# Optimization experiments

Hardware: AMD Instinct MI355X
Metric: run time of the kernel (lower is better)

## Reference

```python
import jax, jax.numpy as jnp
import numpy as np

B, D_W, D_C, D_P = 4096, 2048, 1024, 2048
RANK = D_W // 4  # 512, per A_U/A_V shapes (d_w, d_w//4)


def setup_inputs() -> dict:
    key = jax.random.key(0)
    ks = jax.random.split(key, 10)
    return {
        "w_prev": jax.random.normal(ks[0], (B, D_W), jnp.float32),
        "z_t": jax.random.normal(ks[1], (B, D_P), jnp.float32),
        "c_t": jax.random.normal(ks[2], (B, D_C), jnp.float32),
        # params (mirroring flax init: A_diag zeros, A_U/A_V normal(0.01),
        # Dense kernels lecun_normal-ish scale, zero biases)
        "A_diag": jnp.zeros((D_W,), jnp.float32),
        "A_U": 0.01 * jax.random.normal(ks[3], (D_W, RANK), jnp.float32),
        "A_V": 0.01 * jax.random.normal(ks[4], (D_W, RANK), jnp.float32),
        "W_mod": jax.random.normal(ks[5], (D_C, D_W), jnp.float32) / np.sqrt(D_C),
        "b_mod": jnp.zeros((D_W,), jnp.float32),
        "W_B": jax.random.normal(ks[6], (D_C + D_P, D_W), jnp.float32) / np.sqrt(D_C + D_P),
        "b_B": jnp.zeros((D_W,), jnp.float32),
    }


def reference(w_prev, z_t, c_t, A_diag, A_U, A_V, W_mod, b_mod, W_B, b_B):
    # A = diag(tanh(A_diag)*0.9) + A_U @ A_V^T, row-scaled by modulation.
    # Equivalent (same math) without materializing [B, d_w, d_w]:
    #   (A * m[:, :, None]) @ w = m * (a_diag * w + A_U @ (A_V^T @ w))
    a_diag = jnp.tanh(A_diag) * 0.9                              # [d_w]
    modulation = jnp.tanh(c_t @ W_mod + b_mod)                   # [B, d_w]
    Aw = a_diag * w_prev + (w_prev @ A_V) @ A_U.T                # [B, d_w]
    Bt = jnp.concatenate([c_t, z_t], axis=-1) @ W_B + b_B        # [B, d_w]
    return modulation * Aw + Bt
```

## Files before the change

### kernel.cpp

```cpp
#include <hip/hip_runtime.h>


#define DEV __device__ __forceinline__

typedef __bf16 v8bf __attribute__((ext_vector_type(8)));
typedef __bf16 v4bf __attribute__((ext_vector_type(4)));
typedef float  v4f  __attribute__((ext_vector_type(4)));

typedef __attribute__((address_space(1))) const unsigned int* as1_cuint_ptr;
typedef __attribute__((address_space(3))) unsigned int*       as3_uint_ptr;

DEV void async16(const void* g, void* l) {
  __builtin_amdgcn_global_load_lds(
      (as1_cuint_ptr)(unsigned long long)g,
      (as3_uint_ptr)(unsigned long long)l,
      16, 0, 0);
}

DEV float tanh_fast(float x) {
  x = fminf(15.f, fmaxf(-15.f, x));
  float e = __expf(2.f * x);
  return (e - 1.f) / (e + 1.f);
}

__global__ __launch_bounds__(256, 2) void prep_gemm(
    const float* __restrict__ w, const float* __restrict__ z,
    const float* __restrict__ c, const float* __restrict__ au,
    const float* __restrict__ av, const float* __restrict__ Wmod,
    const float* __restrict__ WB, const float* __restrict__ A_diag,
    __bf16* __restrict__ wb, __bf16* __restrict__ zb, __bf16* __restrict__ cb,
    __bf16* __restrict__ Wmodt, __bf16* __restrict__ WBt,
    __bf16* __restrict__ Mt) {
  __shared__ __align__(16) char smem[16384];
  int b = blockIdx.x;

  if (b < 256) {
    __bf16* As = (__bf16*)smem;
    __bf16* Bs = (__bf16*)(smem + 8192);
    const int tid = threadIdx.x, lane = tid & 63, wid = tid >> 6;
    const int wm = wid >> 1, wn = wid & 1, l16 = lane & 15, quad = lane >> 4;
    const int m0 = (b >> 4) * 128, n0 = (b & 15) * 128;
    const int qs = quad ^ ((l16 >> 1) & 3);
    const int row = tid >> 1, sp = (tid & 1) * 2;

    v4f acc[4][4];
#pragma unroll
    for (int i = 0; i < 4; ++i)
#pragma unroll
      for (int j = 0; j < 4; ++j) { v4f zz = {0, 0, 0, 0}; acc[i][j] = zz; }

    for (int k0 = 0; k0 < 512; k0 += 32) {
      __syncthreads();
#pragma unroll
      for (int ss = 0; ss < 2; ++ss) {
        const int s = sp + ss;
        const int gk = (s ^ ((row >> 1) & 3)) * 8;
        const float* pa = au + (size_t)(m0 + row) * 512 + k0 + gk;
        const float* pb = av + (size_t)(n0 + row) * 512 + k0 + gk;
        float4 a0 = *reinterpret_cast<const float4*>(pa);
        float4 a1 = *reinterpret_cast<const float4*>(pa + 4);
        float4 b0 = *reinterpret_cast<const float4*>(pb);
        float4 b1 = *reinterpret_cast<const float4*>(pb + 4);
        v8bf va, vb;
        va[0] = (__bf16)a0.x; va[1] = (__bf16)a0.y;
        va[2] = (__bf16)a0.z; va[3] = (__bf16)a0.w;
        va[4] = (__bf16)a1.x; va[5] = (__bf16)a1.y;
        va[6] = (__bf16)a1.z; va[7] = (__bf16)a1.w;
        vb[0] = (__bf16)b0.x; vb[1] = (__bf16)b0.y;
        vb[2] = (__bf16)b0.z; vb[3] = (__bf16)b0.w;
        vb[4] = (__bf16)b1.x; vb[5] = (__bf16)b1.y;
        vb[6] = (__bf16)b1.z; vb[7] = (__bf16)b1.w;
        *reinterpret_cast<v8bf*>(&As[row * 32 + s * 8]) = va;
        *reinterpret_cast<v8bf*>(&Bs[row * 32 + s * 8]) = vb;
      }
      __syncthreads();
      const v8bf* Ap = reinterpret_cast<const v8bf*>(As);
      const v8bf* Bp = reinterpret_cast<const v8bf*>(Bs);
      v8bf a[4], bb[4];
#pragma unroll
      for (int i = 0; i < 4; ++i) a[i] = Ap[(wm * 64 + i * 16 + l16) * 4 + qs];
#pragma unroll
      for (int j = 0; j < 4; ++j) bb[j] = Bp[(wn * 64 + j * 16 + l16) * 4 + qs];
#pragma unroll
      for (int i = 0; i < 4; ++i)
#pragma unroll
        for (int j = 0; j < 4; ++j)
          acc[i][j] = __builtin_amdgcn_mfma_f32_16x16x32_bf16(a[i], bb[j],
                                                              acc[i][j], 0, 0, 0);
    }

    const int mBase = m0 + wm * 64 + quad * 4;
    const int nBase = n0 + wn * 64 + l16;
#pragma unroll
    for (int j = 0; j < 4; ++j) {
      const int n = nBase + j * 16;
#pragma unroll
      for (int i = 0; i < 4; ++i)
#pragma unroll
        for (int r = 0; r < 4; ++r) {
          const int m = mBase + i * 16 + r;
          float v = acc[i][j][r];
          if (m == n) v += tanh_fast(A_diag[m]) * 0.9f;
          Mt[(size_t)m * 2048 + n] = (__bf16)v;
        }
    }
    return;
  }

  b -= 256;
  if (b < 2048) {
    for (int u = b; u < 20480; u += 2048) {
      const float* src; __bf16* dst; int off;
      if (u < 8192)       { src = w; dst = wb; off = u; }
      else if (u < 16384) { src = z; dst = zb; off = u - 8192; }
      else                { src = c; dst = cb; off = u - 16384; }
      size_t i = (size_t)off * 1024 + (size_t)threadIdx.x * 4;
      float4 v = *reinterpret_cast<const float4*>(src + i);
      v4bf o;
      o.x = (__bf16)v.x; o.y = (__bf16)v.y;
      o.z = (__bf16)v.z; o.w = (__bf16)v.w;
      *reinterpret_cast<v4bf*>(dst + i) = o;
    }
    return;
  }

  b -= 2048;
  float (*t)[33] = (float(*)[33])smem;
  const int tx = threadIdx.x & 31, ty = threadIdx.x >> 5;
  const int orow = threadIdx.x >> 3;
  const int oc   = (threadIdx.x & 7) * 4;
  for (int u = b; u < 8192; u += 1024) {
    const float* src; __bf16* dst; int R, uu = u;
    if (uu < 2048) { src = Wmod; dst = Wmodt; R = 1024; }
    else           { uu -= 2048; src = WB; dst = WBt; R = 3072; }
    const int c0 = (uu & 63) * 32, r0 = (uu >> 6) * 32;
    const int C = 2048;
    __syncthreads();
#pragma unroll
    for (int rr = 0; rr < 32; rr += 8)
      t[ty + rr][tx] = src[(size_t)(r0 + ty + rr) * C + c0 + tx];
    __syncthreads();
    v4bf o;
    o.x = (__bf16)t[oc + 0][orow];
    o.y = (__bf16)t[oc + 1][orow];
    o.z = (__bf16)t[oc + 2][orow];
    o.w = (__bf16)t[oc + 3][orow];
    *reinterpret_cast<v4bf*>(&dst[(size_t)(c0 + orow) * R + r0 + oc]) = o;
  }
}

__global__ __launch_bounds__(256, 2) void fused_main(
    const __bf16* __restrict__ c, const __bf16* __restrict__ z,
    const __bf16* __restrict__ w, const __bf16* __restrict__ Wmodt,
    const __bf16* __restrict__ Mt, const __bf16* __restrict__ WBt,
    const float* __restrict__ b_mod, const float* __restrict__ b_B,
    float* __restrict__ out) {
  constexpr int DC = 1024, DW = 2048, KB = 3072;
  __shared__ __align__(16) __bf16 As[128 * 128];
  __shared__ __align__(16) __bf16 Bs[128 * 128];

  const int tid = threadIdx.x, lane = tid & 63, wid = tid >> 6;
  const int wm = wid >> 1, wn = wid & 1, l16 = lane & 15, quad = lane >> 4;
  const int flat = blockIdx.y * 16 + blockIdx.x;
  const int swz = (flat & 7) * 64 + (flat >> 3);
  const int m0 = (swz >> 4) * 128;
  const int n0 = (swz & 15) * 128;
  const int r4  = lane >> 4;
  const int s16 = lane & 15;

  v4f acc[4][4];
#pragma unroll
  for (int i = 0; i < 4; ++i)
#pragma unroll
    for (int j = 0; j < 4; ++j) { v4f zz = {0,0,0,0}; acc[i][j] = zz; }

  auto kstep = [&](const __bf16* gA, size_t lda, const __bf16* gB, size_t ldb,
                   int kA, int kB) {
    __syncthreads();
#pragma unroll
    for (int t = 0; t < 8; ++t) {
      const int row = wid * 32 + t * 4 + r4;
      const int gk = (s16 ^ (row & 15)) * 8;
      async16((const void*)(gA + (size_t)(m0 + row) * lda + kA + gk),
              (void*)&As[row * 128 + s16 * 8]);
      async16((const void*)(gB + (size_t)(n0 + row) * ldb + kB + gk),
              (void*)&Bs[row * 128 + s16 * 8]);
    }
    __syncthreads();
    const v8bf* Ap = reinterpret_cast<const v8bf*>(As);
    const v8bf* Bp = reinterpret_cast<const v8bf*>(Bs);
#pragma unroll
    for (int s = 0; s < 4; ++s) {
      const int rs = (s * 4 + quad) ^ l16;
      v8bf a[4], b[4];
#pragma unroll
      for (int i = 0; i < 4; ++i)
        a[i] = Ap[(wm * 64 + i * 16 + l16) * 16 + rs];
#pragma unroll
      for (int j = 0; j < 4; ++j)
        b[j] = Bp[(wn * 64 + j * 16 + l16) * 16 + rs];
#pragma unroll
      for (int i = 0; i < 4; ++i)
#pragma unroll
        for (int j = 0; j < 4; ++j)
          acc[i][j] = __builtin_amdgcn_mfma_f32_16x16x32_bf16(
              a[i], b[j], acc[i][j], 0, 0, 0);
    }
  };

  const int nBase = n0 + wn * 64 + l16;

  for (int k0 = 0; k0 < DC; k0 += 128) kstep(c, DC, Wmodt, DC, k0, k0);

  v4f mod_s[4][4];
#pragma unroll
  for (int j = 0; j < 4; ++j) {
    const float bn = b_mod[nBase + j * 16];
#pragma unroll
    for (int i = 0; i < 4; ++i) {
#pragma unroll
      for (int r = 0; r < 4; ++r)
        mod_s[i][j][r] = tanh_fast(acc[i][j][r] + bn);
      v4f zz = {0,0,0,0};
      acc[i][j] = zz;
    }
  }

  for (int k0 = 0; k0 < DW; k0 += 128) kstep(w, DW, Mt, DW, k0, k0);

#pragma unroll
  for (int i = 0; i < 4; ++i)
#pragma unroll
    for (int j = 0; j < 4; ++j) acc[i][j] *= mod_s[i][j];

  for (int k0 = 0; k0 < DC; k0 += 128) kstep(c, DC, WBt, KB, k0, k0);
  for (int k0 = DC; k0 < KB; k0 += 128) kstep(z, DW, WBt, KB, k0 - DC, k0);

  const int mBase = m0 + wm * 64 + quad * 4;
#pragma unroll
  for (int j = 0; j < 4; ++j) {
    const int n = nBase + j * 16;
    const float bn = b_B[n];
#pragma unroll
    for (int i = 0; i < 4; ++i)
#pragma unroll
      for (int r = 0; r < 4; ++r) {
        const int m = mBase + i * 16 + r;
        out[(size_t)m * DW + n] = acc[i][j][r] + bn;
      }
  }
}


extern "C" void kernel_launch(void* const* d_in, const int* in_sizes, int n_in,
                              void* d_out, int out_size, void* d_ws,
                              size_t ws_size, hipStream_t stream) {
  const float* w_prev = (const float*)d_in[0];
  const float* z_t    = (const float*)d_in[1];
  const float* c_t    = (const float*)d_in[2];
  const float* A_diag = (const float*)d_in[3];
  const float* A_U    = (const float*)d_in[4];
  const float* A_V    = (const float*)d_in[5];
  const float* W_mod  = (const float*)d_in[6];
  const float* b_mod  = (const float*)d_in[7];
  const float* W_B    = (const float*)d_in[8];
  const float* b_B    = (const float*)d_in[9];

  constexpr int Bsz = 4096, DW = 2048;
  const size_t MB = 1ull << 20;
  char* ws = (char*)d_ws;
  __bf16* w_bf  = (__bf16*)(ws + 0);
  __bf16* z_bf  = (__bf16*)(ws + 16 * MB);
  __bf16* c_bf  = (__bf16*)(ws + 32 * MB);
  __bf16* Wmodt = (__bf16*)(ws + 40 * MB);
  __bf16* WBt   = (__bf16*)(ws + 44 * MB);
  __bf16* Mt    = (__bf16*)(ws + 56 * MB);

  prep_gemm<<<3328, 256, 0, stream>>>(w_prev, z_t, c_t, A_U, A_V, W_mod, W_B,
                                      A_diag, w_bf, z_bf, c_bf, Wmodt, WBt,
                                      Mt);

  fused_main<<<dim3(DW / 128, Bsz / 128), 256, 0, stream>>>(
      c_bf, z_bf, w_bf, Wmodt, Mt, WBt, b_mod, b_B, (float*)d_out);
}
```

Baseline: 281.6 us.

## Replace dense A matrix GEMM with low-rank factorized path via w@A_V

After: 315.3 us. +12.0%, slower.

```diff
diff --git a/kernel.cpp b/kernel.cpp
--- a/kernel.cpp
+++ b/kernel.cpp
@@ -27,21 +27,23 @@
     const float* __restrict__ w, const float* __restrict__ z,
     const float* __restrict__ c, const float* __restrict__ au,
     const float* __restrict__ av, const float* __restrict__ Wmod,
-    const float* __restrict__ WB, const float* __restrict__ A_diag,
+    const float* __restrict__ WB,
     __bf16* __restrict__ wb, __bf16* __restrict__ zb, __bf16* __restrict__ cb,
-    __bf16* __restrict__ Wmodt, __bf16* __restrict__ WBt,
-    __bf16* __restrict__ Mt) {
-  __shared__ __align__(16) char smem[16384];
+    __bf16* __restrict__ AUb, __bf16* __restrict__ Wmodt,
+    __bf16* __restrict__ WBt, __bf16* __restrict__ tb) {
+  __shared__ __align__(16) char smem[25600];
   int b = blockIdx.x;
 
-  if (b < 256) {
-    __bf16* As = (__bf16*)smem;
-    __bf16* Bs = (__bf16*)(smem + 8192);
+  if (b < 128) {
+    __bf16* As   = (__bf16*)smem;
+    __bf16* Bs   = (__bf16*)(smem + 8192);
+    __bf16* Braw = (__bf16*)(smem + 16384);
     const int tid = threadIdx.x, lane = tid & 63, wid = tid >> 6;
     const int wm = wid >> 1, wn = wid & 1, l16 = lane & 15, quad = lane >> 4;
-    const int m0 = (b >> 4) * 128, n0 = (b & 15) * 128;
+    const int m0 = (b >> 2) * 128, n0 = (b & 3) * 128;
     const int qs = quad ^ ((l16 >> 1) & 3);
     const int row = tid >> 1, sp = (tid & 1) * 2;
+    const int kk = tid >> 3, nn = (tid & 7) * 16;
 
     v4f acc[4][4];
 #pragma unroll
@@ -49,28 +51,48 @@
 #pragma unroll
       for (int j = 0; j < 4; ++j) { v4f zz = {0, 0, 0, 0}; acc[i][j] = zz; }
 
-    for (int k0 = 0; k0 < 512; k0 += 32) {
+    for (int k0 = 0; k0 < 2048; k0 += 32) {
       __syncthreads();
 #pragma unroll
       for (int ss = 0; ss < 2; ++ss) {
         const int s = sp + ss;
         const int gk = (s ^ ((row >> 1) & 3)) * 8;
-        const float* pa = au + (size_t)(m0 + row) * 512 + k0 + gk;
-        const float* pb = av + (size_t)(n0 + row) * 512 + k0 + gk;
+        const float* pa = w + (size_t)(m0 + row) * 2048 + k0 + gk;
         float4 a0 = *reinterpret_cast<const float4*>(pa);
         float4 a1 = *reinterpret_cast<const float4*>(pa + 4);
-        float4 b0 = *reinterpret_cast<const float4*>(pb);
-        float4 b1 = *reinterpret_cast<const float4*>(pb + 4);
-        v8bf va, vb;
+        v8bf va;
         va[0] = (__bf16)a0.x; va[1] = (__bf16)a0.y;
         va[2] = (__bf16)a0.z; va[3] = (__bf16)a0.w;
         va[4] = (__bf16)a1.x; va[5] = (__bf16)a1.y;
         va[6] = (__bf16)a1.z; va[7] = (__bf16)a1.w;
-        vb[0] = (__bf16)b0.x; vb[1] = (__bf16)b0.y;
-        vb[2] = (__bf16)b0.z; vb[3] = (__bf16)b0.w;
-        vb[4] = (__bf16)b1.x; vb[5] = (__bf16)b1.y;
-        vb[6] = (__bf16)b1.z; vb[7] = (__bf16)b1.w;
         *reinterpret_cast<v8bf*>(&As[row * 32 + s * 8]) = va;
+      }
+      {
+        const float* pb = av + (size_t)(k0 + kk) * 512 + n0 + nn;
+        float4 b0 = *reinterpret_cast<const float4*>(pb);
+        float4 b1 = *reinterpret_cast<const float4*>(pb + 4);
+        float4 b2 = *reinterpret_cast<const float4*>(pb + 8);
+        float4 b3 = *reinterpret_cast<const float4*>(pb + 12);
+        v8bf v0, v1;
+        v0[0] = (__bf16)b0.x; v0[1] = (__bf16)b0.y;
+        v0[2] = (__bf16)b0.z; v0[3] = (__bf16)b0.w;
+        v0[4] = (__bf16)b1.x; v0[5] = (__bf16)b1.y;
+        v0[6] = (__bf16)b1.z; v0[7] = (__bf16)b1.w;
+        v1[0] = (__bf16)b2.x; v1[1] = (__bf16)b2.y;
+        v1[2] = (__bf16)b2.z; v1[3] = (__bf16)b2.w;
+        v1[4] = (__bf16)b3.x; v1[5] = (__bf16)b3.y;
+        v1[6] = (__bf16)b3.z; v1[7] = (__bf16)b3.w;
+        *reinterpret_cast<v8bf*>(&Braw[kk * 130 + nn]) = v0;
+        *reinterpret_cast<v8bf*>(&Braw[kk * 130 + nn + 8]) = v1;
+      }
+      __syncthreads();
+#pragma unroll
+      for (int ss = 0; ss < 2; ++ss) {
+        const int s = sp + ss;
+        const int sg = s ^ ((row >> 1) & 3);
+        v8bf vb;
+#pragma unroll
+        for (int e = 0; e < 8; ++e) vb[e] = Braw[(sg * 8 + e) * 130 + row];
         *reinterpret_cast<v8bf*>(&Bs[row * 32 + s * 8]) = vb;
       }
       __syncthreads();
@@ -97,23 +119,20 @@
 #pragma unroll
       for (int i = 0; i < 4; ++i)
 #pragma unroll
-        for (int r = 0; r < 4; ++r) {
-          const int m = mBase + i * 16 + r;
-          float v = acc[i][j][r];
-          if (m == n) v += tanh_fast(A_diag[m]) * 0.9f;
-          Mt[(size_t)m * 2048 + n] = (__bf16)v;
-        }
+        for (int r = 0; r < 4; ++r)
+          tb[(size_t)(mBase + i * 16 + r) * 512 + n] = (__bf16)acc[i][j][r];
     }
     return;
   }
 
-  b -= 256;
+  b -= 128;
   if (b < 2048) {
-    for (int u = b; u < 20480; u += 2048) {
+    for (int u = b; u < 21504; u += 2048) {
       const float* src; __bf16* dst; int off;
-      if (u < 8192)       { src = w; dst = wb; off = u; }
-      else if (u < 16384) { src = z; dst = zb; off = u - 8192; }
-      else                { src = c; dst = cb; off = u - 16384; }
+      if (u < 8192)       { src = w;  dst = wb;  off = u; }
+      else if (u < 16384) { src = z;  dst = zb;  off = u - 8192; }
+      else if (u < 20480) { src = c;  dst = cb;  off = u - 16384; }
+      else                { src = au; dst = AUb; off = u - 20480; }
       size_t i = (size_t)off * 1024 + (size_t)threadIdx.x * 4;
       float4 v = *reinterpret_cast<const float4*>(src + i);
       v4bf o;
@@ -152,10 +171,11 @@
 __global__ __launch_bounds__(256, 2) void fused_main(
     const __bf16* __restrict__ c, const __bf16* __restrict__ z,
     const __bf16* __restrict__ w, const __bf16* __restrict__ Wmodt,
-    const __bf16* __restrict__ Mt, const __bf16* __restrict__ WBt,
+    const __bf16* __restrict__ tb, const __bf16* __restrict__ AUb,
+    const __bf16* __restrict__ WBt, const float* __restrict__ A_diag,
     const float* __restrict__ b_mod, const float* __restrict__ b_B,
     float* __restrict__ out) {
-  constexpr int DC = 1024, DW = 2048, KB = 3072;
+  constexpr int DC = 1024, DW = 2048, KB = 3072, RK = 512;
   __shared__ __align__(16) __bf16 As[128 * 128];
   __shared__ __align__(16) __bf16 Bs[128 * 128];
 
@@ -209,6 +229,7 @@
   };
 
   const int nBase = n0 + wn * 64 + l16;
+  const int mBase = m0 + wm * 64 + quad * 4;
 
   for (int k0 = 0; k0 < DC; k0 += 128) kstep(c, DC, Wmodt, DC, k0, k0);
 
@@ -226,17 +247,28 @@
     }
   }
 
-  for (int k0 = 0; k0 < DW; k0 += 128) kstep(w, DW, Mt, DW, k0, k0);
-
-#pragma unroll
-  for (int i = 0; i < 4; ++i)
-#pragma unroll
-    for (int j = 0; j < 4; ++j) acc[i][j] *= mod_s[i][j];
+  for (int k0 = 0; k0 < RK; k0 += 128) kstep(tb, RK, AUb, RK, k0, k0);
+
+  {
+    float adr[4];
+#pragma unroll
+    for (int j = 0; j < 4; ++j)
+      adr[j] = tanh_fast(A_diag[nBase + j * 16]) * 0.9f;
+#pragma unroll
+    for (int i = 0; i < 4; ++i)
+#pragma unroll
+      for (int j = 0; j < 4; ++j)
+#pragma unroll
+        for (int r = 0; r < 4; ++r) {
+          const float wv =
+              (float)w[(size_t)(mBase + i * 16 + r) * DW + nBase + j * 16];
+          acc[i][j][r] = (acc[i][j][r] + adr[j] * wv) * mod_s[i][j][r];
+        }
+  }
 
   for (int k0 = 0; k0 < DC; k0 += 128) kstep(c, DC, WBt, KB, k0, k0);
   for (int k0 = DC; k0 < KB; k0 += 128) kstep(z, DW, WBt, KB, k0 - DC, k0);
 
-  const int mBase = m0 + wm * 64 + quad * 4;
 #pragma unroll
   for (int j = 0; j < 4; ++j) {
     const int n = nBase + j * 16;
@@ -274,12 +306,14 @@
   __bf16* c_bf  = (__bf16*)(ws + 32 * MB);
   __bf16* Wmodt = (__bf16*)(ws + 40 * MB);
   __bf16* WBt   = (__bf16*)(ws + 44 * MB);
-  __bf16* Mt    = (__bf16*)(ws + 56 * MB);
-
-  prep_gemm<<<3328, 256, 0, stream>>>(w_prev, z_t, c_t, A_U, A_V, W_mod, W_B,
-                                      A_diag, w_bf, z_bf, c_bf, Wmodt, WBt,
-                                      Mt);
+  __bf16* AUb   = (__bf16*)(ws + 56 * MB);
+  __bf16* t_bf  = (__bf16*)(ws + 58 * MB);
+
+  prep_gemm<<<3200, 256, 0, stream>>>(w_prev, z_t, c_t, A_U, A_V, W_mod, W_B,
+                                      w_bf, z_bf, c_bf, AUb, Wmodt, WBt,
+                                      t_bf);
 
   fused_main<<<dim3(DW / 128, Bsz / 128), 256, 0, stream>>>(
-      c_bf, z_bf, w_bf, Wmodt, Mt, WBt, b_mod, b_B, (float*)d_out);
-}
+      c_bf, z_bf, w_bf, Wmodt, t_bf, AUb, WBt, A_diag, b_mod, b_B,
+      (float*)d_out);
+}
```
